# Kernel optimization log

Measured on AMD Instinct MI355X. Metric: run time of the kernel, lower is better.

The kernel has to match this reference:

```python
import jax, jax.numpy as jnp
import numpy as np

H = 16          # num_heads
D = 64          # head_dim
EPS = 1e-6


def setup_inputs() -> dict:
    key = jax.random.key(0)
    ks = jax.random.split(key, 4)
    B, N, C = 4, 2048, 1024
    x = jax.random.normal(ks[0], (B, N, C), dtype=jnp.float32)
    w_qkv = jax.random.normal(ks[1], (C, 3 * C), dtype=jnp.float32) * (1.0 / np.sqrt(C))
    b_qkv = jnp.zeros((3 * C,), dtype=jnp.float32)
    g_q = jnp.ones((D,), dtype=jnp.float32)
    g_k = jnp.ones((D,), dtype=jnp.float32)
    w_proj = jax.random.normal(ks[2], (C, C), dtype=jnp.float32) * (1.0 / np.sqrt(C))
    b_proj = jnp.zeros((C,), dtype=jnp.float32)
    return {"x": x, "w_qkv": w_qkv, "b_qkv": b_qkv, "g_q": g_q, "g_k": g_k,
            "w_proj": w_proj, "b_proj": b_proj}


def _head_layernorm(t, gamma):
    # LayerNorm over last (head_dim) axis, no bias, with scale. t: [B,H,N,D]
    mu = jnp.mean(t, axis=-1, keepdims=True)
    var = jnp.mean(jnp.square(t - mu), axis=-1, keepdims=True)
    return (t - mu) * jax.lax.rsqrt(var + EPS) * gamma


def reference(x, w_qkv, b_qkv, g_q, g_k, w_proj, b_proj):
    B, N, C = x.shape
    qkv = x @ w_qkv + b_qkv                      # [B, N, 3C]
    qkv = qkv.reshape(B, N, 3, H, D)
    qkv = jnp.transpose(qkv, (2, 0, 3, 1, 4))    # [3, B, H, N, D]
    q, k, v = qkv[0], qkv[1], qkv[2]
    q = _head_layernorm(q, g_q)
    k = _head_layernorm(k, g_k)
    scale = D ** -0.5
    attn = jax.nn.softmax(jnp.einsum('bhqd,bhkd->bhqk', q, k) * scale, axis=-1)
    o = jnp.einsum('bhqk,bhkd->bhqd', attn, v)   # [B, H, N, D]
    o = o.transpose(0, 2, 1, 3).reshape(B, N, C)
    return o @ w_proj + b_proj
```

## Files before the change

kernel.cpp:

```cpp
#include <hip/hip_runtime.h>

#define HH 16
#define DD 64
#define BBATCH 4
#define NSEQ 2048
#define CDIM 1024
#define EPSLN 1e-6f

typedef __bf16 bf16x8 __attribute__((ext_vector_type(8)));
typedef float f32x4 __attribute__((ext_vector_type(4)));
typedef short s16x4 __attribute__((ext_vector_type(4)));
typedef short s16x8 __attribute__((ext_vector_type(8)));
typedef unsigned short u16;

__device__ inline u16 f2b(float f) {
  unsigned u = __builtin_bit_cast(unsigned, f);
  u += 0x7fffu + ((u >> 16) & 1u);
  return (u16)(u >> 16);
}
#if __has_builtin(__builtin_amdgcn_perm)
__device__ inline unsigned pack2(float a, float b) {
  unsigned ua = __builtin_bit_cast(unsigned, a) + 0x8000u;
  unsigned ub = __builtin_bit_cast(unsigned, b) + 0x8000u;
  return __builtin_amdgcn_perm(ub, ua, 0x07060302u);
}
#else
__device__ inline unsigned pack2(float a, float b) {
  unsigned ua = __builtin_bit_cast(unsigned, a);
  unsigned ub = __builtin_bit_cast(unsigned, b);
  return ((ua + 0x8000u) >> 16) | ((ub + 0x8000u) & 0xffff0000u);
}
#endif
#if __has_builtin(__builtin_amdgcn_exp2f)
#define EXP2(x) __builtin_amdgcn_exp2f(x)
#else
#define EXP2(x) __expf((x)*0.6931471805599453f)
#endif

__device__ inline bf16x8 ld_frag16(const u16* p) {
  s16x8 v = *(const s16x8*)p;
  return __builtin_bit_cast(bf16x8, v);
}
__device__ inline f32x4 mfma16(bf16x8 a, bf16x8 b, f32x4 c) {
  return __builtin_amdgcn_mfma_f32_16x16x32_bf16(a, b, c, 0, 0, 0);
}
__device__ inline void async16(const u16* g, u16* l) {
  __builtin_amdgcn_global_load_lds(
      (const __attribute__((address_space(1))) void*)g,
      (__attribute__((address_space(3))) void*)l, 16, 0, 0);
}

__global__ void cvt_x(const float* __restrict__ x, u16* __restrict__ xb) {
  long i = ((long)blockIdx.x * 256 + threadIdx.x) * 8;
  float4 a = *(const float4*)(x + i);
  float4 b = *(const float4*)(x + i + 4);
  u16 r[8];
  r[0] = f2b(a.x); r[1] = f2b(a.y); r[2] = f2b(a.z); r[3] = f2b(a.w);
  r[4] = f2b(b.x); r[5] = f2b(b.y); r[6] = f2b(b.z); r[7] = f2b(b.w);
  *(s16x8*)(xb + i) = *(s16x8*)r;
}

__global__ void cvt_wT(const float* __restrict__ w, u16* __restrict__ wT, int K, int N) {
  __shared__ float tile[32][33];
  int nt = N / 32;
  int bn = blockIdx.x % nt, bk = blockIdx.x / nt;
  int tx = threadIdx.x % 32, ty = threadIdx.x / 32;
  int k0 = bk * 32, n0 = bn * 32;
  for (int j = 0; j < 4; j++)
    tile[ty + 8 * j][tx] = w[(long)(k0 + ty + 8 * j) * N + n0 + tx];
  __syncthreads();
  for (int j = 0; j < 4; j++)
    wT[(long)(n0 + ty + 8 * j) * K + k0 + tx] = f2b(tile[tx][ty + 8 * j]);
}

__launch_bounds__(256, 3)
__global__ void gemm_qkv(const u16* __restrict__ A, const u16* __restrict__ BT,
                         const float* __restrict__ bias,
                         const float* __restrict__ gq, const float* __restrict__ gk,
                         u16* __restrict__ qb, u16* __restrict__ kb, u16* __restrict__ vtb) {
  const int Kd = CDIM;
  __shared__ u16 As[128 * 64];
  __shared__ u16 Bs[128 * 64];
  int t = threadIdx.x;
  int lane = t & 63, wave = t >> 6;
  int ln = lane & 15, quad = lane >> 4;
  int bm = blockIdx.x % 64, bn = blockIdx.x / 64;
  int wm = (wave >> 1) * 64, wn = (wave & 1) * 64;
  int r8 = t >> 3;
  int cb = (t & 7) * 8;
  int cg = (((t & 7) ^ (r8 & 7)) * 8);
  int swl = ln & 7;
  const u16* aB = A + (long)(bm * 128) * Kd + cg;
  const u16* bB = BT + (long)(bn * 128) * Kd + cg;
  f32x4 acc[4][4] = {};
  for (int kt = 0; kt < Kd / 64; kt++) {
    __syncthreads();
#pragma unroll
    for (int c = 0; c < 4; c++) {
      int row = c * 32 + r8;
      async16(aB + (long)row * Kd + kt * 64, As + row * 64 + cb);
      async16(bB + (long)row * Kd + kt * 64, Bs + row * 64 + cb);
    }
    __syncthreads();
#pragma unroll
    for (int kk = 0; kk < 2; kk++) {
      bf16x8 af[4], bfv[4];
#pragma unroll
      for (int mt = 0; mt < 4; mt++)
        af[mt] = ld_frag16(As + (wm + mt * 16 + ln) * 64 + (((kk * 4 + quad) ^ swl) * 8));
#pragma unroll
      for (int nt = 0; nt < 4; nt++)
        bfv[nt] = ld_frag16(Bs + (wn + nt * 16 + ln) * 64 + (((kk * 4 + quad) ^ swl) * 8));
#pragma unroll
      for (int mt = 0; mt < 4; mt++)
#pragma unroll
        for (int nt = 0; nt < 4; nt++)
          acc[mt][nt] = mfma16(af[mt], bfv[nt], acc[mt][nt]);
    }
  }
  int tq = bn >> 3;
  int colbase = bn * 128 + wn;
  int h = (colbase >> 6) & 15;
  int mbase = bm * 128 + wm;
  float bv[4];
#pragma unroll
  for (int nt = 0; nt < 4; nt++) bv[nt] = bias[colbase + nt * 16 + ln];
  if (tq == 2) {
#pragma unroll
    for (int mt = 0; mt < 4; mt++) {
      int m0 = mbase + mt * 16 + quad * 4;
      int b = m0 >> 11, n0 = m0 & 2047;
#pragma unroll
      for (int nt = 0; nt < 4; nt++) {
        int d = nt * 16 + ln;
        u16 pk[4];
#pragma unroll
        for (int r = 0; r < 4; r++) pk[r] = f2b(acc[mt][nt][r] + bv[nt]);
        *(s16x4*)(vtb + ((long)((b * HH + h) * DD + d)) * NSEQ + n0) = *(s16x4*)pk;
      }
    }
  } else {
    const float* g = (tq == 0) ? gq : gk;
    float extra = (tq == 0) ? 0.125f * 1.4426950408889634f : 1.0f;
    u16* dst = (tq == 0) ? qb : kb;
    float gv[4];
#pragma unroll
    for (int nt = 0; nt < 4; nt++) gv[nt] = g[nt * 16 + ln] * extra;
#pragma unroll
    for (int mt = 0; mt < 4; mt++)
#pragma unroll
      for (int r = 0; r < 4; r++) {
        float vv[4];
        float s1 = 0.f, s2 = 0.f;
#pragma unroll
        for (int nt = 0; nt < 4; nt++) {
          vv[nt] = acc[mt][nt][r] + bv[nt];
          s1 += vv[nt];
          s2 += vv[nt] * vv[nt];
        }
#pragma unroll
        for (int m = 1; m < 16; m <<= 1) {
          s1 += __shfl_xor(s1, m);
          s2 += __shfl_xor(s2, m);
        }
        float mu = s1 * (1.0f / 64.0f);
        float var = s2 * (1.0f / 64.0f) - mu * mu;
        float rstd = rsqrtf(var + EPSLN);
        int m = mbase + mt * 16 + quad * 4 + r;
        int b = m >> 11, n = m & 2047;
        long base = ((long)((b * HH + h) * NSEQ + n)) * DD;
#pragma unroll
        for (int nt = 0; nt < 4; nt++)
          dst[base + nt * 16 + ln] = f2b((vv[nt] - mu) * rstd * gv[nt]);
      }
  }
}

__launch_bounds__(256, 2)
__global__ void attn(const u16* __restrict__ qb, const u16* __restrict__ kb,
                     const u16* __restrict__ vtb, u16* __restrict__ ob) {
  __shared__ u16 smem[32768];
  u16* Ks = smem;
  u16* Vs = smem + 8192;
  u16* Pl = smem + 16384;
  int t = threadIdx.x, lane = t & 63, wave = t >> 6;
  int ln = lane & 15, quad = lane >> 4;
  int g = blockIdx.x;
  int bh = (g & 7) * 8 + ((g >> 3) & 7);
  int qblk = (g >> 6) & 7;
  int b = bh >> 4, h = bh & 15;
  const u16* qg = qb + (long)bh * NSEQ * DD;
  const u16* kg = kb + (long)bh * NSEQ * DD;
  const u16* vg = vtb + (long)bh * DD * NSEQ;
  int qrow0 = qblk * 256 + wave * 64;
  bf16x8 bq[4][2];
#pragma unroll
  for (int qf = 0; qf < 4; qf++)
#pragma unroll
    for (int kk = 0; kk < 2; kk++)
      bq[qf][kk] = ld_frag16(qg + (long)(qrow0 + qf * 16 + ln) * DD + kk * 32 + quad * 8);
  f32x4 o[4][4] = {};
  float rs[4] = {0.f, 0.f, 0.f, 0.f};
  u16* Pw = Pl + wave * 4096;
  int psw = (ln & 7) * 8;
  int swl = ln & 7;
  int cK = (lane & 7) ^ (lane >> 3);
  int rV = lane >> 4;
  for (int kv = 0; kv < NSEQ / 128; kv++) {
    __syncthreads();
    long kbase = (long)kv * 128 * DD;
#pragma unroll
    for (int c = 0; c < 4; c++) {
      int rowb = c * 32 + wave * 8;
      async16(kg + kbase + (long)(rowb + (lane >> 3)) * 64 + cK * 8,
              Ks + rowb * 64 + lane * 8);
    }
#pragma unroll
    for (int c = 0; c < 4; c++) {
      int drow = c * 16 + wave * 4;
      int rv = drow + rV;
      int cV = (lane & 15) ^ (rv & 7);
      async16(vg + (long)rv * NSEQ + kv * 128 + cV * 8,
              Vs + drow * 128 + lane * 8);
    }
    __syncthreads();
#pragma unroll
    for (int half = 0; half < 2; half++) {
#pragma unroll
      for (int ctl = 0; ctl < 4; ctl++) {
        int ct = half * 4 + ctl;
        const u16* ka = Ks + (ct * 16 + ln) * 64;
        bf16x8 k0 = ld_frag16(ka + ((quad ^ swl) * 8));
        bf16x8 k1 = ld_frag16(ka + (((quad + 4) ^ swl) * 8));
        int poffc = (ctl * 16 + quad * 4) ^ psw;
#pragma unroll
        for (int qf = 0; qf < 4; qf++) {
          f32x4 z = {};
          z = mfma16(k0, bq[qf][0], z);
          z = mfma16(k1, bq[qf][1], z);
          float e0 = EXP2(z[0]), e1 = EXP2(z[1]), e2 = EXP2(z[2]), e3 = EXP2(z[3]);
          rs[qf] += (e0 + e1) + (e2 + e3);
          uint2 pk;
          pk.x = pack2(e0, e1);
          pk.y = pack2(e2, e3);
          *(uint2*)(Pw + (qf * 16 + ln) * 64 + poffc) = pk;
        }
      }
      bf16x8 pA[4][2];
#pragma unroll
      for (int qf = 0; qf < 4; qf++)
#pragma unroll
        for (int ktl = 0; ktl < 2; ktl++)
          pA[qf][ktl] = ld_frag16(Pw + (qf * 16 + ln) * 64 + ((ktl * 32 + quad * 8) ^ psw));
#pragma unroll
      for (int dt = 0; dt < 4; dt++) {
        const u16* vr = Vs + (dt * 16 + ln) * 128;
#pragma unroll
        for (int ktl = 0; ktl < 2; ktl++) {
          int kt = half * 2 + ktl;
          bf16x8 vv = ld_frag16(vr + (((4 * kt + quad) ^ swl) * 8));
#pragma unroll
          for (int qf = 0; qf < 4; qf++)
            o[qf][dt] = mfma16(pA[qf][ktl], vv, o[qf][dt]);
        }
      }
    }
  }
#pragma unroll
  for (int qf = 0; qf < 4; qf++) {
    float r2 = rs[qf];
    r2 += __shfl_xor(r2, 16);
    r2 += __shfl_xor(r2, 32);
#pragma unroll
    for (int r = 0; r < 4; r++) {
      float inv = 1.0f / __shfl(r2, quad * 4 + r);
      int n = qrow0 + qf * 16 + quad * 4 + r;
      long base = ((long)(b * NSEQ + n) * HH + h) * DD;
#pragma unroll
      for (int dt = 0; dt < 4; dt++)
        ob[base + dt * 16 + ln] = f2b(o[qf][dt][r] * inv);
    }
  }
}

__launch_bounds__(256, 3)
__global__ void gemm_proj(const u16* __restrict__ A, const u16* __restrict__ BT,
                          const float* __restrict__ bias, float* __restrict__ out) {
  const int Kd = CDIM;
  __shared__ u16 As[128 * 64];
  __shared__ u16 Bs[128 * 64];
  int t = threadIdx.x;
  int lane = t & 63, wave = t >> 6;
  int ln = lane & 15, quad = lane >> 4;
  int bm = blockIdx.x % 64, bn = blockIdx.x / 64;
  int wm = (wave >> 1) * 64, wn = (wave & 1) * 64;
  int r8 = t >> 3;
  int cb = (t & 7) * 8;
  int cg = (((t & 7) ^ (r8 & 7)) * 8);
  int swl = ln & 7;
  const u16* aB = A + (long)(bm * 128) * Kd + cg;
  const u16* bB = BT + (long)(bn * 128) * Kd + cg;
  f32x4 acc[4][4] = {};
  for (int kt = 0; kt < Kd / 64; kt++) {
    __syncthreads();
#pragma unroll
    for (int c = 0; c < 4; c++) {
      int row = c * 32 + r8;
      async16(aB + (long)row * Kd + kt * 64, As + row * 64 + cb);
      async16(bB + (long)row * Kd + kt * 64, Bs + row * 64 + cb);
    }
    __syncthreads();
#pragma unroll
    for (int kk = 0; kk < 2; kk++) {
      bf16x8 af[4], bfv[4];
#pragma unroll
      for (int mt = 0; mt < 4; mt++)
        af[mt] = ld_frag16(As + (wm + mt * 16 + ln) * 64 + (((kk * 4 + quad) ^ swl) * 8));
#pragma unroll
      for (int nt = 0; nt < 4; nt++)
        bfv[nt] = ld_frag16(Bs + (wn + nt * 16 + ln) * 64 + (((kk * 4 + quad) ^ swl) * 8));
#pragma unroll
      for (int mt = 0; mt < 4; mt++)
#pragma unroll
        for (int nt = 0; nt < 4; nt++)
          acc[mt][nt] = mfma16(af[mt], bfv[nt], acc[mt][nt]);
    }
  }
#pragma unroll
  for (int mt = 0; mt < 4; mt++)
#pragma unroll
    for (int nt = 0; nt < 4; nt++) {
      int col = bn * 128 + wn + nt * 16 + ln;
      float bvx = bias[col];
#pragma unroll
      for (int r = 0; r < 4; r++) {
        int m = bm * 128 + wm + mt * 16 + quad * 4 + r;
        out[(long)m * CDIM + col] = acc[mt][nt][r] + bvx;
      }
    }
}

extern "C" void kernel_launch(void* const* d_in, const int* in_sizes, int n_in,
                              void* d_out, int out_size, void* d_ws, size_t ws_size,
                              hipStream_t stream) {
  const float* x = (const float*)d_in[0];
  const float* w_qkv = (const float*)d_in[1];
  const float* b_qkv = (const float*)d_in[2];
  const float* g_q = (const float*)d_in[3];
  const float* g_k = (const float*)d_in[4];
  const float* w_proj = (const float*)d_in[5];
  const float* b_proj = (const float*)d_in[6];
  float* out = (float*)d_out;

  char* ws = (char*)d_ws;
  const size_t MB = 1024 * 1024;
  u16* xb = (u16*)ws;
  u16* wqkvT = (u16*)(ws + 16 * MB);
  u16* wprojT = (u16*)(ws + 22 * MB);
  u16* qb = (u16*)(ws + 24 * MB);
  u16* kb = (u16*)(ws + 40 * MB);
  u16* vtb = (u16*)(ws + 56 * MB);
  u16* ob = xb;

  cvt_x<<<4096, 256, 0, stream>>>(x, xb);
  cvt_wT<<<(1024 / 32) * (3072 / 32), 256, 0, stream>>>(w_qkv, wqkvT, CDIM, 3 * CDIM);
  cvt_wT<<<(1024 / 32) * (1024 / 32), 256, 0, stream>>>(w_proj, wprojT, CDIM, CDIM);
  gemm_qkv<<<64 * 24, 256, 0, stream>>>(xb, wqkvT, b_qkv, g_q, g_k, qb, kb, vtb);
  attn<<<512, 256, 0, stream>>>(qb, kb, vtb, ob);
  gemm_proj<<<64 * 8, 256, 0, stream>>>(ob, wprojT, b_proj, out);
}
```

Baseline: 259.1 us.

## Prefetch next K/V tile into registers while computing current attention tile

Replaces the per-iteration async global-to-LDS loads with a register-staged software pipeline. The first K/V tile is loaded before the loop, and each iteration issues global loads for the next tile into registers, runs the QK/PV MFMA work, then writes the registers to LDS after a barrier. The aim is to hide global memory latency behind compute. It also raises wave priority around the PV MFMA block. The cost is higher register pressure, which may lower occupancy, and an extra LDS store pass per tile.

```diff
diff --git a/kernel.cpp b/kernel.cpp
--- a/kernel.cpp
+++ b/kernel.cpp
@@ -206,24 +206,38 @@
   int swl = ln & 7;
   int cK = (lane & 7) ^ (lane >> 3);
   int rV = lane >> 4;
+
+  int lr3 = lane >> 3;
+  const u16* kpfB = kg + (long)(wave * 8 + lr3) * DD + cK * 8;
+  int cV = (lane & 15) ^ ((wave * 4 + rV) & 7);
+  const u16* vpfB = vg + (long)(wave * 4 + rV) * NSEQ + cV * 8;
+  u16* kdst = Ks + wave * 8 * 64 + lane * 8;
+  u16* vdst = Vs + wave * 4 * 128 + lane * 8;
+
+#pragma unroll
+  for (int c = 0; c < 4; c++) {
+    int rowb = c * 32 + wave * 8;
+    async16(kg + (long)(rowb + lr3) * DD + cK * 8, Ks + rowb * 64 + lane * 8);
+  }
+#pragma unroll
+  for (int c = 0; c < 4; c++) {
+    int drow = c * 16 + wave * 4;
+    int rv = drow + rV;
+    async16(vg + (long)rv * NSEQ + cV * 8, Vs + drow * 128 + lane * 8);
+  }
+  __syncthreads();
+
+  uint4 krg[4], vrg[4];
   for (int kv = 0; kv < NSEQ / 128; kv++) {
-    __syncthreads();
-    long kbase = (long)kv * 128 * DD;
-#pragma unroll
-    for (int c = 0; c < 4; c++) {
-      int rowb = c * 32 + wave * 8;
-      async16(kg + kbase + (long)(rowb + (lane >> 3)) * 64 + cK * 8,
-              Ks + rowb * 64 + lane * 8);
-    }
-#pragma unroll
-    for (int c = 0; c < 4; c++) {
-      int drow = c * 16 + wave * 4;
-      int rv = drow + rV;
-      int cV = (lane & 15) ^ (rv & 7);
-      async16(vg + (long)rv * NSEQ + kv * 128 + cV * 8,
-              Vs + drow * 128 + lane * 8);
-    }
-    __syncthreads();
+    bool pf = (kv + 1) < (NSEQ / 128);
+    if (pf) {
+      const u16* ks = kpfB + (long)(kv + 1) * 128 * DD;
+      const u16* vs = vpfB + (long)(kv + 1) * 128;
+#pragma unroll
+      for (int c = 0; c < 4; c++) krg[c] = *(const uint4*)(ks + c * 32 * DD);
+#pragma unroll
+      for (int c = 0; c < 4; c++) vrg[c] = *(const uint4*)(vs + (long)c * 16 * NSEQ);
+    }
 #pragma unroll
     for (int half = 0; half < 2; half++) {
 #pragma unroll
@@ -254,16 +268,26 @@
           pA[qf][ktl] = ld_frag16(Pw + (qf * 16 + ln) * 64 + ((ktl * 32 + quad * 8) ^ psw));
 #pragma unroll
       for (int dt = 0; dt < 4; dt++) {
-        const u16* vr = Vs + (dt * 16 + ln) * 128;
+        const u16* vrow = Vs + (dt * 16 + ln) * 128;
+        __builtin_amdgcn_s_setprio(1);
 #pragma unroll
         for (int ktl = 0; ktl < 2; ktl++) {
           int kt = half * 2 + ktl;
-          bf16x8 vv = ld_frag16(vr + (((4 * kt + quad) ^ swl) * 8));
+          bf16x8 vv = ld_frag16(vrow + (((4 * kt + quad) ^ swl) * 8));
 #pragma unroll
           for (int qf = 0; qf < 4; qf++)
             o[qf][dt] = mfma16(pA[qf][ktl], vv, o[qf][dt]);
         }
-      }
+        __builtin_amdgcn_s_setprio(0);
+      }
+    }
+    __syncthreads();
+    if (pf) {
+#pragma unroll
+      for (int c = 0; c < 4; c++) *(uint4*)(kdst + c * 32 * 64) = krg[c];
+#pragma unroll
+      for (int c = 0; c < 4; c++) *(uint4*)(vdst + c * 16 * 128) = vrg[c];
+      __syncthreads();
     }
   }
 #pragma unroll
```

Result: slower. 362.1 us (+39.8%).
